# Kernel optimization log

Measured on AMD Instinct MI355X. Metric: run time of the kernel, lower is better.

## Reference

```python
import jax, jax.numpy as jnp
import numpy as np

WSIZE = 8
HEADS = 6
CYC_SHIFT = True


def _relative_index(w):
    # same math as SelfAttention._getRelativeIndex
    coords = np.stack(np.meshgrid(np.arange(w), np.arange(w), indexing='ij'))
    coords = coords.reshape(2, -1)                      # [2, w*w]
    rel = coords[:, :, None] - coords[:, None, :]       # [2, N, N]
    rel = rel.copy()
    rel[0] += w - 1
    rel[0] *= 2 * w - 1
    rel[1] += w - 1
    return (rel[0] + rel[1]).reshape(-1)                # [N*N]


def _shift_mask(H, W, w):
    # same math as CycShftWndwPartition._mask
    part = np.zeros((H, W), dtype=np.float32)
    slices = [slice(0, -w), slice(-w, -w // 2), slice(-w // 2, None)]
    idx = 0
    for hs in slices:
        for ws_ in slices:
            part[hs, ws_] = idx
            idx += 1
    part = part.reshape(H // w, w, W // w, w).transpose(0, 2, 1, 3).reshape(-1, w * w)
    diff = part[:, None, :] - part[:, :, None]          # [nW, N, N]
    return np.where(diff != 0, -100.0, 0.0).astype(np.float32)


def setup_inputs() -> dict:
    key = jax.random.key(0)
    k0, k1, k2, k3, k4 = jax.random.split(key, 5)
    B, H, W, C = 4, 384, 384, 60
    return {
        'cvrt_img': jax.random.normal(k0, (B, H, W, C), dtype=jnp.float32),
        'qkv_w': jax.random.normal(k1, (C, 3 * C), dtype=jnp.float32) * 0.05,
        'bias_matrix': jax.random.normal(k2, ((2 * WSIZE - 1) ** 2, HEADS), dtype=jnp.float32) * 0.02,
        'proj_w': jax.random.normal(k3, (C, C), dtype=jnp.float32) * 0.05,
        'proj_b': jax.random.normal(k4, (C,), dtype=jnp.float32) * 0.02,
    }


def reference(cvrt_img, qkv_w, bias_matrix, proj_w, proj_b):
    B, H, W, C = cvrt_img.shape
    w = WSIZE
    N = w * w
    d = C // HEADS
    nWh, nWw = H // w, W // w
    WNum = nWh * nWw

    # cyclic shift + window partition
    if CYC_SHIFT:
        x = jnp.roll(cvrt_img, shift=(-(w // 2), -(w // 2)), axis=(1, 2))
        mask = jnp.asarray(_shift_mask(H, W, w))        # [WNum, N, N]
    else:
        x = cvrt_img
        mask = jnp.zeros((WNum, N, N), dtype=cvrt_img.dtype)
    windows = x.reshape(B, nWh, w, nWw, w, C).transpose(0, 1, 3, 2, 4, 5)
    windows = windows.reshape(B * WNum, N, C)

    # windowed multi-head self-attention
    qkv = (windows @ qkv_w).reshape(B * WNum, N, 3, HEADS, d)
    qkv = qkv.transpose(2, 0, 3, 1, 4)                  # [3, Bw, H, N, d]
    q, k, v = qkv[0], qkv[1], qkv[2]
    attn = jnp.einsum('bhnd,bhmd->bhnm', q, k) / (d ** 0.5)

    rel_idx = jnp.asarray(_relative_index(w))
    bias = bias_matrix[rel_idx].reshape(N, N, HEADS).transpose(2, 0, 1)  # [H, N, N]
    attn = attn + bias[None]

    attn = attn.reshape(B, WNum, HEADS, N, N) + mask[None, :, None]
    attn = jax.nn.softmax(attn.reshape(B * WNum, HEADS, N, N), axis=-1)

    out = jnp.einsum('bhnm,bhmd->bhnd', attn, v)        # [Bw, H, N, d]
    out = out.transpose(0, 2, 1, 3).reshape(B * WNum, N, C)
    new_windows = out @ proj_w + proj_b

    # un-partition + reverse cyclic shift
    y = new_windows.reshape(B, nWh, nWw, w, w, C).transpose(0, 1, 3, 2, 4, 5)
    y = y.reshape(B, H, W, C)
    if CYC_SHIFT:
        y = jnp.roll(y, shift=(w // 2, w // 2), axis=(1, 2))
    return y
```

## Files before the change

### kernel.cpp

```cpp
#include <hip/hip_runtime.h>
#include <hip/hip_bf16.h>

#define IMG    384
#define CDIM   60
#define NWIN   48
#define WNUM   (NWIN * NWIN)

typedef short  bf16x8 __attribute__((ext_vector_type(8)));
typedef float  f32x4  __attribute__((ext_vector_type(4)));
union Frag { int4 i4; bf16x8 b8; };

#define MFMA(a, b, c) __builtin_amdgcn_mfma_f32_16x16x32_bf16((a), (b), (c), 0, 0, 0)

#define WS_QKVF  0
#define WS_VF    24576
#define WS_PROJF 36864
#define WS_BIASF 45056

#define SCALE_L2E (0.31622776601683794f * 1.4426950408889634f)
#define MASK_L2E  144.26950408889634f
#define LOG2E     1.4426950408889634f

__device__ __forceinline__ unsigned short f2bf(float f) {
    unsigned int u = __float_as_uint(f);
    unsigned int r = u + 0x7fffu + ((u >> 16) & 1u);
    return (unsigned short)(r >> 16);
}
__device__ __forceinline__ unsigned int pk2bf(float a, float b) {
    union { __hip_bfloat162 h; unsigned int u; } c;
    c.h = __float22bfloat162_rn(float2{a, b});
    return c.u;
}
__device__ __forceinline__ int regionOf(int x) {
    return (x < IMG - 8) ? 0 : ((x < IMG - 4) ? 1 : 2);
}
__device__ __forceinline__ int qk_byte(int tok, int byteoff) {
    return (tok * 192 + byteoff) ^ ((tok & 7) << 4);
}

__global__ void swin_prep(const float* __restrict__ qw,
                          const float* __restrict__ pw,
                          const float* __restrict__ bias,
                          unsigned char* __restrict__ ws)
{
    int t = blockIdx.x * 256 + threadIdx.x;
    if (t < 1536) {
        int lane = t & 63, f = t >> 6;
        int mt = f >> 1, ks = f & 1;
        int h = mt >> 1, type = mt & 1;
        int d = lane & 15, g8 = lane >> 4;
        unsigned short v8[8];
        #pragma unroll
        for (int jj = 0; jj < 8; ++jj) {
            int c = ks * 32 + g8 * 8 + jj;
            v8[jj] = f2bf((d < 10 && c < 60) ? qw[c * 180 + type * 60 + h * 10 + d] : 0.f);
        }
        int4 p;
        p.x = v8[0] | (v8[1] << 16);  p.y = v8[2] | (v8[3] << 16);
        p.z = v8[4] | (v8[5] << 16);  p.w = v8[6] | (v8[7] << 16);
        *(int4*)(ws + WS_QKVF + t * 16) = p;
    } else if (t < 2304) {
        int t2 = t - 1536;
        int lane = t2 & 63, f = t2 >> 6;
        int h = f >> 1, ks = f & 1;
        int d = lane & 15, g8 = lane >> 4;
        unsigned short v8[8];
        #pragma unroll
        for (int jj = 0; jj < 8; ++jj) {
            int c = ks * 32 + g8 * 8 + jj;
            v8[jj] = f2bf((d < 10 && c < 60) ? qw[c * 180 + 120 + h * 10 + d] : 0.f);
        }
        int4 p;
        p.x = v8[0] | (v8[1] << 16);  p.y = v8[2] | (v8[3] << 16);
        p.z = v8[4] | (v8[5] << 16);  p.w = v8[6] | (v8[7] << 16);
        *(int4*)(ws + WS_VF + t2 * 16) = p;
    } else if (t < 2816) {
        int t2 = t - 2304;
        int lane = t2 & 63, fq = t2 >> 6;
        int m = fq >> 1, ks = fq & 1;
        int c = m * 16 + (lane & 15);
        int g8 = lane >> 4;
        unsigned short v8[8];
        #pragma unroll
        for (int jj = 0; jj < 8; ++jj) {
            int cc = ks * 32 + g8 * 8 + jj;
            v8[jj] = f2bf((c < 60 && cc < 60) ? pw[cc * 60 + c] : 0.f);
        }
        int4 p;
        p.x = v8[0] | (v8[1] << 16);  p.y = v8[2] | (v8[3] << 16);
        p.z = v8[4] | (v8[5] << 16);  p.w = v8[6] | (v8[7] << 16);
        *(int4*)(ws + WS_PROJF + t2 * 16) = p;
    } else if (t < 2816 + 24576) {
        int idx = t - 2816;
        int h = idx >> 12, r = idx & 4095;
        int i = r >> 6, j = r & 63;
        int yi = i >> 3, xi = i & 7, yj = j >> 3, xj = j & 7;
        int ridx = (yi - yj + 7) * 15 + (xi - xj + 7);
        ((float*)(ws + WS_BIASF))[h * 4096 + i * 64 + j] = bias[ridx * 6 + h] * LOG2E;
    }
}

__global__ __launch_bounds__(256, 3)
void swin_mfma(const float* __restrict__ img,
               const float* __restrict__ pbias,
               const unsigned char* __restrict__ ws,
               float* __restrict__ out)
{
    __shared__ unsigned short uni [64 * 72];
    __shared__ unsigned short qall[64 * 96];
    __shared__ unsigned short kall[64 * 96];
    __shared__ unsigned short vall[66 * 72];
    __shared__ unsigned short osb [64 * 72];
    __shared__ __align__(16) int zfrag[4];

    const int tid  = threadIdx.x;
    const int lane = tid & 63;
    const int wid  = __builtin_amdgcn_readfirstlane(tid >> 6);
    const int l15  = lane & 15;
    const int g    = lane >> 4;
    const bool zg  = (lane >= 32);
    const int dl   = (32 + l15) << 2;

    const int bid = blockIdx.x;
    const int b   = bid / WNUM;
    const int wi  = bid - b * WNUM;
    const int wh  = wi / NWIN;
    const int ww  = wi - wh * NWIN;
    const bool boundary = (wh == NWIN - 1) || (ww == NWIN - 1);

    {
        int tok = lane;
        int yi = tok >> 3, xi = tok & 7;
        int sh = wh * 8 + yi + 4; if (sh >= IMG) sh -= IMG;
        int sw = ww * 8 + xi + 4; if (sw >= IMG) sw -= IMG;
        const float* src = img + ((size_t)(b * IMG + sh) * IMG + sw) * CDIM;
        #pragma unroll
        for (int it = 0; it < 4; ++it) {
            int cg = wid + it * 4;
            if (cg < 15) {
                float4 v = *(const float4*)(src + cg * 4);
                *(int2*)&uni[tok * 72 + cg * 4] =
                    make_int2(pk2bf(v.x, v.y), pk2bf(v.z, v.w));
            } else {
                *(int2*)&uni[tok * 72 + 60] = make_int2(0, 0);
            }
        }
    }
    if (tid < 128) {
        int row = tid >> 1, half = tid & 1;
        *(unsigned int*)&osb[row * 72 + 60 + half * 2] = 0u;
    }
    if (tid < 192) {
        int h = tid >> 5, s = tid & 31;
        ((unsigned int*)vall)[((h * 11 + 10) * 72 >> 1) + s] = 0x3F803F80u;
    }
    if (tid < 4) zfrag[tid] = 0;
    __syncthreads();

    {
        Frag xb[4][2];
        #pragma unroll
        for (int n = 0; n < 4; ++n)
            #pragma unroll
            for (int ks = 0; ks < 2; ++ks)
                xb[n][ks].i4 = *(const int4*)&uni[(n * 16 + l15) * 72 + ks * 32 + g * 8];

        const int4* wsq = (const int4*)(ws + WS_QKVF);
        #pragma unroll
        for (int kk = 0; kk < 3; ++kk) {
            int mt = wid + kk * 4;
            int h = mt >> 1, type = mt & 1;
            Frag a0, a1;
            a0.i4 = wsq[(mt * 2 + 0) * 64 + lane];
            a1.i4 = wsq[(mt * 2 + 1) * 64 + lane];
            unsigned short* dst = type ? kall : qall;
            #pragma unroll
            for (int n = 0; n < 4; ++n) {
                f32x4 acc = {0.f, 0.f, 0.f, 0.f};
                acc = MFMA(a0.b8, xb[n][0].b8, acc);
                acc = MFMA(a1.b8, xb[n][1].b8, acc);
                int tok = n * 16 + l15;
                *(int2*)((char*)dst + qk_byte(tok, h * 32 + g * 8)) =
                    make_int2(pk2bf(acc[0], acc[1]), pk2bf(acc[2], acc[3]));
            }
        }
        const int4* wsv = (const int4*)(ws + WS_VF);
        int nv = (wid < 2) ? 2 : 1;
        #pragma unroll 1
        for (int kk = 0; kk < nv; ++kk) {
            int hv = wid + kk * 4;
            Frag a0, a1;
            a0.i4 = wsv[(hv * 2 + 0) * 64 + lane];
            a1.i4 = wsv[(hv * 2 + 1) * 64 + lane];
            #pragma unroll
            for (int n = 0; n < 4; ++n) {
                f32x4 acc = {0.f, 0.f, 0.f, 0.f};
                acc = MFMA(a0.b8, xb[n][0].b8, acc);
                acc = MFMA(a1.b8, xb[n][1].b8, acc);
                int tok = n * 16 + l15;
                #pragma unroll
                for (int jj = 0; jj < 4; ++jj) {
                    int d = g * 4 + jj;
                    if (d < 10) vall[(hv * 11 + d) * 72 + tok] = f2bf(acc[jj]);
                }
            }
        }
    }
    __syncthreads();

    unsigned short* pslab = &uni[wid * 16 * 72];
    const float* biasf = (const float*)(ws + WS_BIASF);

    int h  = wid + (wid >> 1);
    int m0 = (wid & 1) * 2;
    int mc = 4 - (wid & 1) * 2;
    #pragma unroll 1
    for (int grp = 0; grp < 2; ++grp) {
        const int koff = h * 32 + (g & 1) * 16;
        Frag kb[4];
        #pragma unroll
        for (int n = 0; n < 4; ++n) {
            int tok = n * 16 + l15;
            const int4* pa = zg ? (const int4*)zfrag
                                : (const int4*)((const char*)kall + qk_byte(tok, koff));
            kb[n].i4 = *pa;
        }
        int vrow = (l15 < 10) ? l15 : 10;
        Frag va[2];
        #pragma unroll
        for (int ks = 0; ks < 2; ++ks)
            va[ks].i4 = *(const int4*)&vall[(h * 11 + vrow) * 72 + ks * 32 + g * 8];

        #pragma unroll 1
        for (int m = m0; m < m0 + mc; ++m) {
            int i_tok = m * 16 + l15;
            Frag qa;
            {
                const int4* pa = zg ? (const int4*)zfrag
                                    : (const int4*)((const char*)qall + qk_byte(i_tok, koff));
                qa.i4 = *pa;
            }
            f32x4 sacc[4];
            #pragma unroll
            for (int n = 0; n < 4; ++n) {
                f32x4 zz = {0.f, 0.f, 0.f, 0.f};
                sacc[n] = MFMA(kb[n].b8, qa.b8, zz);
            }
            const float* bp = biasf + ((h << 6) + i_tok) * 64;
            float p[4][4];
            #pragma unroll
            for (int n = 0; n < 4; ++n) {
                float4 bb = *(const float4*)(bp + n * 16 + (g << 2));
                p[n][0] = fmaf(sacc[n][0], SCALE_L2E, bb.x);
                p[n][1] = fmaf(sacc[n][1], SCALE_L2E, bb.y);
                p[n][2] = fmaf(sacc[n][2], SCALE_L2E, bb.z);
                p[n][3] = fmaf(sacc[n][3], SCALE_L2E, bb.w);
            }
            if (boundary) {
                int pi = regionOf(wh * 8 + (i_tok >> 3)) * 3 + regionOf(ww * 8 + (i_tok & 7));
                #pragma unroll
                for (int n = 0; n < 4; ++n)
                    #pragma unroll
                    for (int jj = 0; jj < 4; ++jj) {
                        int j = n * 16 + g * 4 + jj;
                        int pj = regionOf(wh * 8 + (j >> 3)) * 3 + regionOf(ww * 8 + (j & 7));
                        if (pi != pj) p[n][jj] -= MASK_L2E;
                    }
            }
            #pragma unroll
            for (int n = 0; n < 4; ++n) {
                float e0 = __builtin_exp2f(p[n][0]);
                float e1 = __builtin_exp2f(p[n][1]);
                float e2 = __builtin_exp2f(p[n][2]);
                float e3 = __builtin_exp2f(p[n][3]);
                *(int2*)&pslab[l15 * 72 + n * 16 + g * 4] =
                    make_int2(pk2bf(e0, e1), pk2bf(e2, e3));
            }
            f32x4 pv = {0.f, 0.f, 0.f, 0.f};
            #pragma unroll
            for (int ks = 0; ks < 2; ++ks) {
                Frag pb2;
                pb2.i4 = *(const int4*)&pslab[l15 * 72 + ks * 32 + g * 8];
                pv = MFMA(va[ks].b8, pb2.b8, pv);
            }
            float denom = __int_as_float(__builtin_amdgcn_ds_bpermute(dl, __float_as_int(pv[2])));
            float rinv  = __builtin_amdgcn_rcpf(denom);

            int base = i_tok * 72 + h * 10;
            if (g == 0) {
                *(unsigned int*)&osb[base + 0] = pk2bf(pv[0] * rinv, pv[1] * rinv);
                *(unsigned int*)&osb[base + 2] = pk2bf(pv[2] * rinv, pv[3] * rinv);
            } else if (g == 1) {
                *(unsigned int*)&osb[base + 4] = pk2bf(pv[0] * rinv, pv[1] * rinv);
                *(unsigned int*)&osb[base + 6] = pk2bf(pv[2] * rinv, pv[3] * rinv);
            } else if (g == 2) {
                *(unsigned int*)&osb[base + 8] = pk2bf(pv[0] * rinv, pv[1] * rinv);
            }
        }
        h += 1; m0 = 0; mc = 6 - mc;
    }
    __syncthreads();

    {
        const int4* wsp = (const int4*)(ws + WS_PROJF);
        Frag a0, a1;
        a0.i4 = wsp[(wid * 2 + 0) * 64 + lane];
        a1.i4 = wsp[(wid * 2 + 1) * 64 + lane];
        int c0 = wid * 16 + g * 4;
        float4 pbv = (c0 < 60) ? *(const float4*)&pbias[c0] : float4{0.f, 0.f, 0.f, 0.f};
        #pragma unroll
        for (int n = 0; n < 4; ++n) {
            Frag b0, b1;
            b0.i4 = *(const int4*)&osb[(n * 16 + l15) * 72 + g * 8];
            b1.i4 = *(const int4*)&osb[(n * 16 + l15) * 72 + 32 + g * 8];
            f32x4 acc = {0.f, 0.f, 0.f, 0.f};
            acc = MFMA(a0.b8, b0.b8, acc);
            acc = MFMA(a1.b8, b1.b8, acc);
            if (c0 < 60) {
                int tok = n * 16 + l15;
                int yi = tok >> 3, xi = tok & 7;
                int sh = wh * 8 + yi + 4; if (sh >= IMG) sh -= IMG;
                int sw = ww * 8 + xi + 4; if (sw >= IMG) sw -= IMG;
                float4 o = {acc[0] + pbv.x, acc[1] + pbv.y, acc[2] + pbv.z, acc[3] + pbv.w};
                *(float4*)&out[((b * IMG + sh) * IMG + sw) * CDIM + c0] = o;
            }
        }
    }
}

extern "C" void kernel_launch(void* const* d_in, const int* in_sizes, int n_in,
                              void* d_out, int out_size, void* d_ws, size_t ws_size,
                              hipStream_t stream) {
    const float* img  = (const float*)d_in[0];
    const float* qw   = (const float*)d_in[1];
    const float* bias = (const float*)d_in[2];
    const float* pw   = (const float*)d_in[3];
    const float* pb   = (const float*)d_in[4];
    float* out = (float*)d_out;

    swin_prep<<<107, 256, 0, stream>>>(qw, pw, bias, (unsigned char*)d_ws);
    swin_mfma<<<4 * WNUM, 256, 0, stream>>>(img, pb,
                                            (const unsigned char*)d_ws, out);
}
```

Before: 190.9 us.

## Compact shared-memory tiles to 128-byte swizzled rows and raise occupancy target

Replaces the padded 72- and 96-element shared-memory rows with unpadded 64-element rows addressed through an XOR swizzle. Q/K storage is packed tighter, with the extra head dimensions placed in a tail region, and V is produced by swapped MFMA operands so it lands transposed in rows. The smaller LDS footprint lets launch bounds request 4 blocks per CU instead of 3, aiming for better latency hiding. The cost is more complex fragment addressing and branchy partial loads, and the V prep relies on the workspace layout matching the swapped operand roles.

```diff
diff --git a/kernel.cpp b/kernel.cpp
--- a/kernel.cpp
+++ b/kernel.cpp
@@ -34,8 +34,16 @@
 __device__ __forceinline__ int regionOf(int x) {
     return (x < IMG - 8) ? 0 : ((x < IMG - 4) ? 1 : 2);
 }
-__device__ __forceinline__ int qk_byte(int tok, int byteoff) {
-    return (tok * 192 + byteoff) ^ ((tok & 7) << 4);
+__device__ __forceinline__ int swz(int row, int byteoff) {
+    return (row * 128 + byteoff) ^ ((row & 7) << 4);
+}
+__device__ __forceinline__ int4 qk_frag(const unsigned short* buf, int tok, int h, int g) {
+    if (g == 0) return *(const int4*)((const char*)buf + swz(tok, h * 16));
+    if (g == 1) {
+        int v = *(const int*)((const char*)buf + swz(tok, 96 + h * 4));
+        return int4{v, 0, 0, 0};
+    }
+    return int4{0, 0, 0, 0};
 }
 
 __global__ void swin_prep(const float* __restrict__ qw,
@@ -100,25 +108,23 @@
     }
 }
 
-__global__ __launch_bounds__(256, 3)
+__global__ __launch_bounds__(256, 4)
 void swin_mfma(const float* __restrict__ img,
                const float* __restrict__ pbias,
                const unsigned char* __restrict__ ws,
                float* __restrict__ out)
 {
-    __shared__ unsigned short uni [64 * 72];
-    __shared__ unsigned short qall[64 * 96];
-    __shared__ unsigned short kall[64 * 96];
-    __shared__ unsigned short vall[66 * 72];
-    __shared__ unsigned short osb [64 * 72];
-    __shared__ __align__(16) int zfrag[4];
+    __shared__ __align__(16) unsigned short uni [64 * 64];
+    __shared__ __align__(16) unsigned short qall[64 * 64];
+    __shared__ __align__(16) unsigned short kall[64 * 64];
+    __shared__ __align__(16) unsigned short vall[61 * 64];
+    __shared__ __align__(16) unsigned short osb [64 * 64];
 
     const int tid  = threadIdx.x;
     const int lane = tid & 63;
     const int wid  = __builtin_amdgcn_readfirstlane(tid >> 6);
     const int l15  = lane & 15;
     const int g    = lane >> 4;
-    const bool zg  = (lane >= 32);
     const int dl   = (32 + l15) << 2;
 
     const int bid = blockIdx.x;
@@ -139,22 +145,20 @@
             int cg = wid + it * 4;
             if (cg < 15) {
                 float4 v = *(const float4*)(src + cg * 4);
-                *(int2*)&uni[tok * 72 + cg * 4] =
+                *(int2*)((char*)uni + swz(tok, cg * 8)) =
                     make_int2(pk2bf(v.x, v.y), pk2bf(v.z, v.w));
             } else {
-                *(int2*)&uni[tok * 72 + 60] = make_int2(0, 0);
+                *(int2*)((char*)uni + swz(tok, 120)) = make_int2(0, 0);
             }
         }
     }
     if (tid < 128) {
         int row = tid >> 1, half = tid & 1;
-        *(unsigned int*)&osb[row * 72 + 60 + half * 2] = 0u;
-    }
-    if (tid < 192) {
-        int h = tid >> 5, s = tid & 31;
-        ((unsigned int*)vall)[((h * 11 + 10) * 72 >> 1) + s] = 0x3F803F80u;
-    }
-    if (tid < 4) zfrag[tid] = 0;
+        *(unsigned int*)((char*)osb + swz(row, 120 + half * 4)) = 0u;
+    }
+    if (tid < 32) {
+        *(unsigned int*)((char*)vall + swz(60, tid * 4)) = 0x3F803F80u;
+    }
     __syncthreads();
 
     {
@@ -163,7 +167,7 @@
         for (int n = 0; n < 4; ++n)
             #pragma unroll
             for (int ks = 0; ks < 2; ++ks)
-                xb[n][ks].i4 = *(const int4*)&uni[(n * 16 + l15) * 72 + ks * 32 + g * 8];
+                xb[n][ks].i4 = *(const int4*)((const char*)uni + swz(n * 16 + l15, ks * 64 + g * 16));
 
         const int4* wsq = (const int4*)(ws + WS_QKVF);
         #pragma unroll
@@ -180,8 +184,12 @@
                 acc = MFMA(a0.b8, xb[n][0].b8, acc);
                 acc = MFMA(a1.b8, xb[n][1].b8, acc);
                 int tok = n * 16 + l15;
-                *(int2*)((char*)dst + qk_byte(tok, h * 32 + g * 8)) =
-                    make_int2(pk2bf(acc[0], acc[1]), pk2bf(acc[2], acc[3]));
+                unsigned pk01 = pk2bf(acc[0], acc[1]);
+                unsigned pk23 = pk2bf(acc[2], acc[3]);
+                if (g < 2)
+                    *(int2*)((char*)dst + swz(tok, h * 16 + g * 8)) = make_int2(pk01, pk23);
+                else if (g == 2)
+                    *(unsigned*)((char*)dst + swz(tok, 96 + h * 4)) = pk01;
             }
         }
         const int4* wsv = (const int4*)(ws + WS_VF);
@@ -189,26 +197,24 @@
         #pragma unroll 1
         for (int kk = 0; kk < nv; ++kk) {
             int hv = wid + kk * 4;
-            Frag a0, a1;
-            a0.i4 = wsv[(hv * 2 + 0) * 64 + lane];
-            a1.i4 = wsv[(hv * 2 + 1) * 64 + lane];
+            Frag b0, b1;
+            b0.i4 = wsv[(hv * 2 + 0) * 64 + lane];
+            b1.i4 = wsv[(hv * 2 + 1) * 64 + lane];
             #pragma unroll
             for (int n = 0; n < 4; ++n) {
                 f32x4 acc = {0.f, 0.f, 0.f, 0.f};
-                acc = MFMA(a0.b8, xb[n][0].b8, acc);
-                acc = MFMA(a1.b8, xb[n][1].b8, acc);
-                int tok = n * 16 + l15;
-                #pragma unroll
-                for (int jj = 0; jj < 4; ++jj) {
-                    int d = g * 4 + jj;
-                    if (d < 10) vall[(hv * 11 + d) * 72 + tok] = f2bf(acc[jj]);
+                acc = MFMA(xb[n][0].b8, b0.b8, acc);
+                acc = MFMA(xb[n][1].b8, b1.b8, acc);
+                if (l15 < 10) {
+                    *(int2*)((char*)vall + swz(hv * 10 + l15, n * 32 + g * 8)) =
+                        make_int2(pk2bf(acc[0], acc[1]), pk2bf(acc[2], acc[3]));
                 }
             }
         }
     }
     __syncthreads();
 
-    unsigned short* pslab = &uni[wid * 16 * 72];
+    const int prow = wid * 16 + l15;
     const float* biasf = (const float*)(ws + WS_BIASF);
 
     int h  = wid + (wid >> 1);
@@ -216,30 +222,22 @@
     int mc = 4 - (wid & 1) * 2;
     #pragma unroll 1
     for (int grp = 0; grp < 2; ++grp) {
-        const int koff = h * 32 + (g & 1) * 16;
         Frag kb[4];
         #pragma unroll
-        for (int n = 0; n < 4; ++n) {
-            int tok = n * 16 + l15;
-            const int4* pa = zg ? (const int4*)zfrag
-                                : (const int4*)((const char*)kall + qk_byte(tok, koff));
-            kb[n].i4 = *pa;
-        }
-        int vrow = (l15 < 10) ? l15 : 10;
+        for (int n = 0; n < 4; ++n)
+            kb[n].i4 = qk_frag(kall, n * 16 + l15, h, g);
+        int vrow = (l15 < 10) ? h * 10 + l15 : 60;
         Frag va[2];
         #pragma unroll
         for (int ks = 0; ks < 2; ++ks)
-            va[ks].i4 = *(const int4*)&vall[(h * 11 + vrow) * 72 + ks * 32 + g * 8];
+            va[ks].i4 = *(const int4*)((const char*)vall + swz(vrow, ks * 64 + g * 16));
 
         #pragma unroll 1
         for (int m = m0; m < m0 + mc; ++m) {
             int i_tok = m * 16 + l15;
             Frag qa;
-            {
-                const int4* pa = zg ? (const int4*)zfrag
-                                    : (const int4*)((const char*)qall + qk_byte(i_tok, koff));
-                qa.i4 = *pa;
-            }
+            qa.i4 = qk_frag(qall, i_tok, h, g);
+
             f32x4 sacc[4];
             #pragma unroll
             for (int n = 0; n < 4; ++n) {
@@ -273,28 +271,26 @@
                 float e1 = __builtin_exp2f(p[n][1]);
                 float e2 = __builtin_exp2f(p[n][2]);
                 float e3 = __builtin_exp2f(p[n][3]);
-                *(int2*)&pslab[l15 * 72 + n * 16 + g * 4] =
+                *(int2*)((char*)uni + swz(prow, n * 32 + g * 8)) =
                     make_int2(pk2bf(e0, e1), pk2bf(e2, e3));
             }
             f32x4 pv = {0.f, 0.f, 0.f, 0.f};
             #pragma unroll
             for (int ks = 0; ks < 2; ++ks) {
                 Frag pb2;
-                pb2.i4 = *(const int4*)&pslab[l15 * 72 + ks * 32 + g * 8];
+                pb2.i4 = *(const int4*)((const char*)uni + swz(prow, ks * 64 + g * 16));
                 pv = MFMA(va[ks].b8, pb2.b8, pv);
             }
             float denom = __int_as_float(__builtin_amdgcn_ds_bpermute(dl, __float_as_int(pv[2])));
             float rinv  = __builtin_amdgcn_rcpf(denom);
 
-            int base = i_tok * 72 + h * 10;
-            if (g == 0) {
-                *(unsigned int*)&osb[base + 0] = pk2bf(pv[0] * rinv, pv[1] * rinv);
-                *(unsigned int*)&osb[base + 2] = pk2bf(pv[2] * rinv, pv[3] * rinv);
-            } else if (g == 1) {
-                *(unsigned int*)&osb[base + 4] = pk2bf(pv[0] * rinv, pv[1] * rinv);
-                *(unsigned int*)&osb[base + 6] = pk2bf(pv[2] * rinv, pv[3] * rinv);
+            unsigned q01 = pk2bf(pv[0] * rinv, pv[1] * rinv);
+            unsigned q23 = pk2bf(pv[2] * rinv, pv[3] * rinv);
+            if (g < 2) {
+                *(unsigned*)((char*)osb + swz(i_tok, h * 20 + g * 8 + 0)) = q01;
+                *(unsigned*)((char*)osb + swz(i_tok, h * 20 + g * 8 + 4)) = q23;
             } else if (g == 2) {
-                *(unsigned int*)&osb[base + 8] = pk2bf(pv[0] * rinv, pv[1] * rinv);
+                *(unsigned*)((char*)osb + swz(i_tok, h * 20 + 16)) = q01;
             }
         }
         h += 1; m0 = 0; mc = 6 - mc;
@@ -311,8 +307,8 @@
         #pragma unroll
         for (int n = 0; n < 4; ++n) {
             Frag b0, b1;
-            b0.i4 = *(const int4*)&osb[(n * 16 + l15) * 72 + g * 8];
-            b1.i4 = *(const int4*)&osb[(n * 16 + l15) * 72 + 32 + g * 8];
+            b0.i4 = *(const int4*)((const char*)osb + swz(n * 16 + l15, g * 16));
+            b1.i4 = *(const int4*)((const char*)osb + swz(n * 16 + l15, 64 + g * 16));
             f32x4 acc = {0.f, 0.f, 0.f, 0.f};
             acc = MFMA(a0.b8, b0.b8, acc);
             acc = MFMA(a1.b8, b1.b8, acc);
```

Result: faster. 180.7 us (-5.3%).
